# Optimization experiments

Hardware: AMD Instinct MI355X
Metric: run time of the kernel (lower is better)

The kernel has to match this reference:

```python
import jax, jax.numpy as jnp
import numpy as np

G = 8            # group_order
KS = 3           # kernel size
C1, O1 = 1, 16   # gconv1 channels
C2, O2 = 16, 32  # gconv2 channels
HW = 28
NUM_CLASSES = 10


def _bilinear_sample(img, px, py):
    # img: (O, I, K, K); px, py: (K, K) pixel coords; zero padding outside
    # (matches torch grid_sample bilinear, align_corners=False, padding_mode='zeros')
    K = img.shape[-1]
    x0 = jnp.floor(px); y0 = jnp.floor(py)
    wx = px - x0; wy = py - y0
    x0i = x0.astype(jnp.int32); y0i = y0.astype(jnp.int32)

    def gather(yi, xi):
        valid = (yi >= 0) & (yi < K) & (xi >= 0) & (xi < K)
        yc = jnp.clip(yi, 0, K - 1)
        xc = jnp.clip(xi, 0, K - 1)
        return img[:, :, yc, xc] * valid.astype(img.dtype)  # (O,I,K,K)

    return (gather(y0i, x0i) * (1 - wx) * (1 - wy)
            + gather(y0i, x0i + 1) * wx * (1 - wy)
            + gather(y0i + 1, x0i) * (1 - wx) * wy
            + gather(y0i + 1, x0i + 1) * wx * wy)


def _rotated_kernels(base, group_order):
    # Replicates F.affine_grid + F.grid_sample (align_corners=False) for each rotation k.
    K = base.shape[-1]
    coords = (2.0 * jnp.arange(K, dtype=base.dtype) + 1.0) / K - 1.0  # normalized centers
    xs, ys = jnp.meshgrid(coords, coords, indexing='xy')  # x along width, y along height

    def rot_k(k):
        theta = 2.0 * np.pi * k / group_order
        c, s = jnp.cos(theta), jnp.sin(theta)
        gx = c * xs - s * ys   # theta row [cos, -sin, 0]
        gy = s * xs + c * ys   # theta row [sin,  cos, 0]
        px = ((gx + 1.0) * K - 1.0) / 2.0  # unnormalize, align_corners=False
        py = ((gy + 1.0) * K - 1.0) / 2.0
        return _bilinear_sample(base, px, py)

    return jax.vmap(rot_k)(jnp.arange(group_order, dtype=base.dtype))  # (G,O,I,K,K)


def _conv2d(x, w, pad):
    return jax.lax.conv_general_dilated(
        x, w, window_strides=(1, 1), padding=[(pad, pad), (pad, pad)],
        dimension_numbers=('NCHW', 'OIHW', 'NCHW'))


def setup_inputs() -> dict:
    key = jax.random.key(0)
    k1, k2, k3, k4, k5 = jax.random.split(key, 5)
    x = jax.random.normal(k1, (512, C1, HW, HW), dtype=jnp.float32)
    base_weight = jax.random.normal(k2, (O1, C1, KS, KS), dtype=jnp.float32)
    w2 = jax.random.normal(k3, (O2, C2, G, KS, KS), dtype=jnp.float32) * 0.05
    fc_w = jax.random.normal(k4, (NUM_CLASSES, O2 * HW * HW), dtype=jnp.float32) * 0.01
    fc_b = jax.random.normal(k5, (NUM_CLASSES,), dtype=jnp.float32) * 0.01
    return {"x": x, "base_weight": base_weight, "w2": w2, "fc_w": fc_w, "fc_b": fc_b}


def reference(x, base_weight, w2, fc_w, fc_b):
    B = x.shape[0]
    # --- GroupConv2D: steerable rotated kernels, concat along out-channels (k-major) ---
    rk = _rotated_kernels(base_weight, G)           # (G, O1, C1, K, K)
    w1 = rk.reshape(G * O1, C1, KS, KS)
    h = _conv2d(x, w1, 1)                           # (B, G*O1, 28, 28)
    h = jax.nn.relu(h)                              # GroupReLU == plain ReLU

    # --- GroupToGroupConv: circulant structure fused into one conv ---
    # torch: out channel = g*O2 + o (cat dim=1), in channel = c*G + h_idx (view layout)
    g = jnp.arange(G)[:, None]
    hh = jnp.arange(G)[None, :]
    idx = (g - hh) % G                               # (G, G)
    Wc = w2[:, :, idx]                               # (O2, C2, G_g, G_h, K, K)
    Wbig = jnp.transpose(Wc, (2, 0, 1, 3, 4, 5)).reshape(G * O2, C2 * G, KS, KS)
    h2 = _conv2d(h, Wbig, 1)                         # (B, G*O2, 28, 28)
    h2 = jax.nn.relu(h2)

    # --- GroupPooling (mean over the *inner* factor of 8, as in the torch view) ---
    p = h2.reshape(B, (G * O2) // G, G, HW, HW).mean(axis=2)  # (B, 32, 28, 28)

    # --- fc ---
    flat = p.reshape(B, -1)
    return flat @ fc_w.T + fc_b
```

## Files before the change

kernel.cpp:

```cpp
#include <hip/hip_runtime.h>
#include <hip/hip_bf16.h>
#include <cstdint>

#define AS1 __attribute__((address_space(1)))
#define AS3 __attribute__((address_space(3)))

typedef __bf16 bf16x8 __attribute__((ext_vector_type(8)));
typedef float  f32x16 __attribute__((ext_vector_type(16)));

__device__ __forceinline__ void gld_lds16(const void* g, void* l) {
    __builtin_amdgcn_global_load_lds((const AS1 void*)g, (AS3 void*)l, 16, 0, 0);
}

__global__ void k_rot(const float* __restrict__ base, float* __restrict__ w1) {
    int m = threadIdx.x;
    int g = m >> 4, o = m & 15;
    float th = 6.28318530717958647692f * (float)g / 8.0f;
    float c = cosf(th), s = sinf(th);
    for (int i = 0; i < 3; ++i) {
        float ys = (2.0f * i + 1.0f) / 3.0f - 1.0f;
        for (int j = 0; j < 3; ++j) {
            float xs = (2.0f * j + 1.0f) / 3.0f - 1.0f;
            float gx = c * xs - s * ys;
            float gy = s * xs + c * ys;
            float px = ((gx + 1.0f) * 3.0f - 1.0f) * 0.5f;
            float py = ((gy + 1.0f) * 3.0f - 1.0f) * 0.5f;
            float x0 = floorf(px), y0 = floorf(py);
            float wx = px - x0, wy = py - y0;
            int x0i = (int)x0, y0i = (int)y0;
            auto gat = [&](int yi, int xi) -> float {
                bool v = (yi >= 0) && (yi < 3) && (xi >= 0) && (xi < 3);
                int yc = min(max(yi, 0), 2), xc = min(max(xi, 0), 2);
                return v ? base[o * 9 + yc * 3 + xc] : 0.0f;
            };
            w1[m * 9 + i * 3 + j] =
                  gat(y0i, x0i)         * (1.0f - wx) * (1.0f - wy)
                + gat(y0i, x0i + 1)     * wx          * (1.0f - wy)
                + gat(y0i + 1, x0i)     * (1.0f - wx) * wy
                + gat(y0i + 1, x0i + 1) * wx          * wy;
        }
    }
}

__global__ __launch_bounds__(256) void k_conv1(const float* __restrict__ x,
                                               const float* __restrict__ w1g,
                                               const float* __restrict__ w2,
                                               __hip_bfloat16* __restrict__ hl,
                                               __hip_bfloat16* __restrict__ A) {
    int tid = threadIdx.x;

    if (blockIdx.x < 1152) {
        int i = blockIdx.x * 256 + tid;
        int r = i / 1152, k = i - r * 1152;
        int g = r >> 5, o2 = r & 31;
        int kk = k >> 7, cch = k & 127;
        int ky = kk / 3, kx = kk - ky * 3;
        int c2 = cch >> 3, hh = cch & 7;
        int gi = (g - hh) & 7;
        A[i] = __float2bfloat16(w2[((o2 * 16 + c2) * 8 + gi) * 9 + ky * 3 + kx]);
    }

    __shared__ float w1s[1152];
    for (int i = tid; i < 1152; i += 256) w1s[i] = w1g[i];
    __syncthreads();

    const int c0 = (tid & 15) * 8;
    float wreg[8][9];
#pragma unroll
    for (int cc = 0; cc < 8; ++cc)
#pragma unroll
        for (int k = 0; k < 9; ++k) wreg[cc][k] = w1s[(c0 + cc) * 9 + k];

    const int slot = tid >> 4;
    const int band = blockIdx.x % 15;
    const int b    = blockIdx.x / 15;
    const int yy   = band * 2 + (slot >> 3);
    const int xx0  = (slot & 7) * 4;

    const float* xb = x + b * 784;
    float xv[3][6];
#pragma unroll
    for (int t = 0; t < 3; ++t) {
        int sy = yy - 2 + t;
        bool syok = (sy >= 0) && (sy < 28);
#pragma unroll
        for (int u = 0; u < 6; ++u) {
            int sx = xx0 - 2 + u;
            bool ok = syok && (sx >= 0) && (sx < 28);
            xv[t][u] = ok ? xb[sy * 28 + sx] : 0.0f;
        }
    }

    float acc[4][8];
#pragma unroll
    for (int j = 0; j < 4; ++j)
#pragma unroll
        for (int cc = 0; cc < 8; ++cc) acc[j][cc] = 0.0f;

#pragma unroll
    for (int t = 0; t < 3; ++t)
#pragma unroll
        for (int u = 0; u < 3; ++u) {
#pragma unroll
            for (int j = 0; j < 4; ++j) {
                float xvv = xv[t][j + u];
#pragma unroll
                for (int cc = 0; cc < 8; ++cc)
                    acc[j][cc] += xvv * wreg[cc][t * 3 + u];
            }
        }

#pragma unroll
    for (int j = 0; j < 4; ++j) {
        int xx = xx0 + j;
        if (xx < 30) {
            bool interior = (yy >= 1) && (yy <= 28) && (xx >= 1) && (xx <= 28);
            union { __hip_bfloat16 h[8]; float4 f4; } u;
#pragma unroll
            for (int cc = 0; cc < 8; ++cc)
                u.h[cc] = __float2bfloat16(interior ? fmaxf(acc[j][cc], 0.0f) : 0.0f);
            int pi = b * 900 + yy * 30 + xx;
            *(float4*)(hl + (size_t)pi * 128 + c0) = u.f4;
        }
    }
}

__global__ __launch_bounds__(256, 4) void k_conv2(const __hip_bfloat16* __restrict__ A,
                                                  const __hip_bfloat16* __restrict__ hl,
                                                  __hip_bfloat16* __restrict__ p) {
    __shared__ __align__(16) char smem[32768];

    const int tid  = threadIdx.x;
    const int lane = tid & 63;
    const int w    = tid >> 6;
    const int wr   = w >> 1, wc = w & 1;
    const int hi   = lane >> 5;

    const int bid  = blockIdx.x;
    const int xcd  = bid & 7;
    const int slot = bid >> 3;
    const int nt   = xcd + 8 * (slot >> 1);
    const int mt   = slot & 1;
    const int n0 = nt << 7;
    const int r0 = mt << 7;

    uint32_t aG[4], bG[4], ldsOff[4];
#pragma unroll
    for (int q = 0; q < 4; ++q) {
        int ch = w * 4 + q;
        int rl = ch * 8 + (lane >> 3);
        int ca = (lane & 7) ^ (rl & 7) ^ (ch & 3);
        aG[q] = (uint32_t)((r0 + rl) * 2304 + ca * 16);
        int n  = n0 + rl;
        int b  = n / 784; int rr = n - b * 784;
        int y  = rr / 28; int xx = rr - y * 28;
        bG[q]  = (uint32_t)(((b * 30 + y) * 30 + xx) * 256 + ca * 16);
        ldsOff[q] = (uint32_t)(ch * 1024);
    }

    uint32_t aro[2], bro[2]; int asw[2], bsw[2];
#pragma unroll
    for (int t = 0; t < 2; ++t) {
        int rl = 64 * wr + 32 * t + (lane & 31);
        aro[t] = (uint32_t)(rl * 128); asw[t] = (rl & 7) ^ ((rl >> 3) & 3);
        int nl = 64 * wc + 32 * t + (lane & 31);
        bro[t] = (uint32_t)(16384 + nl * 128); bsw[t] = (nl & 7) ^ ((nl >> 3) & 3);
    }

    f32x16 acc[2][2];
#pragma unroll
    for (int i = 0; i < 2; ++i)
#pragma unroll
        for (int j = 0; j < 2; ++j) acc[i][j] = (f32x16)(0.0f);

    const char* Ab = (const char*)A;
    const char* Hb = (const char*)hl;

    for (int s = 0; s < 18; ++s) {
        int kk = s >> 1, half = s & 1;
        int ky = kk / 3, kx = kk - ky * 3;
        int aoff = kk * 256 + half * 128;
        int boff = (ky * 30 + kx) * 256 + half * 128;

        __syncthreads();
#pragma unroll
        for (int q = 0; q < 4; ++q) {
            gld_lds16(Ab + aG[q] + aoff, smem + ldsOff[q]);
            gld_lds16(Hb + bG[q] + boff, smem + 16384 + ldsOff[q]);
        }
        __syncthreads();

#pragma unroll
        for (int kstep = 0; kstep < 4; ++kstep) {
            int cb = kstep * 2 + hi;
            bf16x8 af[2], bf[2];
#pragma unroll
            for (int t = 0; t < 2; ++t) {
                af[t] = *(const bf16x8*)(smem + aro[t] + ((cb ^ asw[t]) * 16));
                bf[t] = *(const bf16x8*)(smem + bro[t] + ((cb ^ bsw[t]) * 16));
            }
#pragma unroll
            for (int i = 0; i < 2; ++i)
#pragma unroll
                for (int j = 0; j < 2; ++j)
                    acc[i][j] = __builtin_amdgcn_mfma_f32_32x32x16_bf16(af[i], bf[j], acc[i][j], 0, 0, 0);
        }
    }

#pragma unroll
    for (int ti = 0; ti < 2; ++ti) {
        int gbase = (r0 + 64 * wr + 32 * ti) >> 3;
#pragma unroll
        for (int tj = 0; tj < 2; ++tj) {
            f32x16 v = acc[ti][tj];
#pragma unroll
            for (int q = 0; q < 4; ++q) {
                float s = fmaxf(v[4*q], 0.0f) + fmaxf(v[4*q+1], 0.0f)
                        + fmaxf(v[4*q+2], 0.0f) + fmaxf(v[4*q+3], 0.0f);
                s += __shfl_xor(s, 32, 64);
                if (hi == 0) {
                    int a = gbase + q;
                    int n = n0 + 64 * wc + 32 * tj + (lane & 31);
                    int b = n / 784; int rr = n - b * 784;
                    p[(b * 32 + a) * 784 + rr] = __float2bfloat16(s * 0.125f);
                }
            }
        }
    }
}

__global__ __launch_bounds__(256) void k_fc(const __hip_bfloat16* __restrict__ p,
                                            const float* __restrict__ fw,
                                            const float* __restrict__ fb,
                                            float* __restrict__ out) {
    int b = blockIdx.x >> 2, ks = blockIdx.x & 3;
    int tid = threadIdx.x;
    const bf16x8* pb = (const bf16x8*)(p + (size_t)b * 25088);
    const float4* w4 = (const float4*)fw;
    float acc[10] = {};
    for (int t = ks * 784 + tid; t < (ks + 1) * 784; t += 256) {
        union { bf16x8 v; __hip_bfloat16 h[8]; } u;
        u.v = pb[t];
        float vf[8];
#pragma unroll
        for (int e = 0; e < 8; ++e) vf[e] = __bfloat162float(u.h[e]);
#pragma unroll
        for (int c = 0; c < 10; ++c) {
            float4 u0 = w4[c * 6272 + 2 * t];
            float4 u1 = w4[c * 6272 + 2 * t + 1];
            acc[c] += vf[0] * u0.x + vf[1] * u0.y + vf[2] * u0.z + vf[3] * u0.w
                    + vf[4] * u1.x + vf[5] * u1.y + vf[6] * u1.z + vf[7] * u1.w;
        }
    }
    __shared__ float red[10][4];
    int lane = tid & 63, wv = tid >> 6;
#pragma unroll
    for (int c = 0; c < 10; ++c) {
        float s = acc[c];
#pragma unroll
        for (int o = 32; o > 0; o >>= 1) s += __shfl_down(s, o, 64);
        if (lane == 0) red[c][wv] = s;
    }
    __syncthreads();
    if (tid < 10) {
        float s = red[tid][0] + red[tid][1] + red[tid][2] + red[tid][3];
        if (ks == 0) s += fb[tid];
        atomicAdd(&out[b * 10 + tid], s);
    }
}

extern "C" void kernel_launch(void* const* d_in, const int* in_sizes, int n_in,
                              void* d_out, int out_size, void* d_ws, size_t ws_size,
                              hipStream_t stream) {
    const float* x  = (const float*)d_in[0];
    const float* bw = (const float*)d_in[1];
    const float* w2 = (const float*)d_in[2];
    const float* fw = (const float*)d_in[3];
    const float* fb = (const float*)d_in[4];
    float* out = (float*)d_out;
    char* ws = (char*)d_ws;

    float*          w1   = (float*)(ws);
    __hip_bfloat16* Amat = (__hip_bfloat16*)(ws + 4608);
    __hip_bfloat16* hl   = (__hip_bfloat16*)(ws + 594432);
    __hip_bfloat16* p    = (__hip_bfloat16*)(ws + 118563328);

    hipMemsetAsync(d_out, 0, (size_t)out_size * sizeof(float), stream);
    k_rot  <<<1,    128, 0, stream>>>(bw, w1);
    k_conv1<<<7680, 256, 0, stream>>>(x, w1, w2, hl, Amat);
    k_conv2<<<6272, 256, 0, stream>>>(Amat, hl, p);
    k_fc   <<<2048, 256, 0, stream>>>(p, fw, fb, out);
}
```

Before: 371.9 us.

## Restructure conv2 GEMM into 256x256 tiles with double-buffered LDS pipeline

Rewrites the second group convolution GEMM so each 512-thread block computes a 256x256 output tile, covering all output channels for 256 pixels. It double-buffers 128KB of LDS and splits each K step into four quadrant phases, so global-to-LDS loads of the next step overlap the MFMAs of the current one. It also uses s_setprio around the MFMA bursts. The larger tile means the pixel operand is fetched once instead of twice, and the pipeline hides load latency that the old two-barrier loop exposed. In exchange, the big LDS footprint limits occupancy and the hand-placed waitcnt/barrier sequencing is fragile.

New measurement: 377.1 us. No clear change (+1.4%).

```diff
diff --git a/kernel.cpp b/kernel.cpp
--- a/kernel.cpp
+++ b/kernel.cpp
@@ -125,104 +125,242 @@
     }
 }
 
-__global__ __launch_bounds__(256, 4) void k_conv2(const __hip_bfloat16* __restrict__ A,
+__global__ __launch_bounds__(512, 2) void k_conv2(const __hip_bfloat16* __restrict__ A,
                                                   const __hip_bfloat16* __restrict__ hl,
                                                   __hip_bfloat16* __restrict__ p) {
-    __shared__ __align__(16) char smem[32768];
+    __shared__ __align__(16) char smem[131072];
 
     const int tid  = threadIdx.x;
     const int lane = tid & 63;
     const int w    = tid >> 6;
-    const int wr   = w >> 1, wc = w & 1;
     const int hi   = lane >> 5;
-
-    const int bid  = blockIdx.x;
-    const int xcd  = bid & 7;
-    const int slot = bid >> 3;
-    const int nt   = xcd + 8 * (slot >> 1);
-    const int mt   = slot & 1;
-    const int n0 = nt << 7;
-    const int r0 = mt << 7;
-
-    uint32_t aG[4], bG[4], ldsOff[4];
-#pragma unroll
-    for (int q = 0; q < 4; ++q) {
-        int ch = w * 4 + q;
+    const int wqr  = w >> 2;
+    const int wqc  = w & 3;
+
+    const int bid = blockIdx.x;
+    const int nt  = (bid & 7) * 196 + (bid >> 3);
+    const int n0  = nt << 8;
+
+    uint32_t aSrc[2], bSrc[2][2], ldsCh[2];
+#pragma unroll
+    for (int q = 0; q < 2; ++q) {
+        int ch = 2 * w + q;
         int rl = ch * 8 + (lane >> 3);
         int ca = (lane & 7) ^ (rl & 7) ^ (ch & 3);
-        aG[q] = (uint32_t)((r0 + rl) * 2304 + ca * 16);
-        int n  = n0 + rl;
-        int b  = n / 784; int rr = n - b * 784;
-        int y  = rr / 28; int xx = rr - y * 28;
-        bG[q]  = (uint32_t)(((b * 30 + y) * 30 + xx) * 256 + ca * 16);
-        ldsOff[q] = (uint32_t)(ch * 1024);
-    }
-
-    uint32_t aro[2], bro[2]; int asw[2], bsw[2];
-#pragma unroll
-    for (int t = 0; t < 2; ++t) {
-        int rl = 64 * wr + 32 * t + (lane & 31);
-        aro[t] = (uint32_t)(rl * 128); asw[t] = (rl & 7) ^ ((rl >> 3) & 3);
-        int nl = 64 * wc + 32 * t + (lane & 31);
-        bro[t] = (uint32_t)(16384 + nl * 128); bsw[t] = (nl & 7) ^ ((nl >> 3) & 3);
-    }
-
-    f32x16 acc[2][2];
-#pragma unroll
-    for (int i = 0; i < 2; ++i)
-#pragma unroll
-        for (int j = 0; j < 2; ++j) acc[i][j] = (f32x16)(0.0f);
+        aSrc[q]  = (uint32_t)(rl * 2304 + ca * 16);
+        ldsCh[q] = (uint32_t)(ch * 1024);
+#pragma unroll
+        for (int hn = 0; hn < 2; ++hn) {
+            int n = n0 + hn * 128 + rl;
+            int b = n / 784; int rr = n - b * 784;
+            int y = rr / 28; int xx = rr - y * 28;
+            bSrc[q][hn] = (uint32_t)(((b * 30 + y) * 30 + xx) * 256 + ca * 16);
+        }
+    }
+
+    uint32_t aRow[2]; int aSwz[2];
+#pragma unroll
+    for (int i = 0; i < 2; ++i) {
+        int r = wqr * 64 + i * 32 + (lane & 31);
+        aRow[i] = (uint32_t)(r * 128);
+        aSwz[i] = (r & 7) ^ ((r >> 3) & 3);
+    }
+    const int rB = wqc * 32 + (lane & 31);
+    const uint32_t bRow = (uint32_t)(rB * 128);
+    const int bSwz = (rB & 7) ^ ((rB >> 3) & 3);
+
+    f32x16 acc[4][2];
+#pragma unroll
+    for (int pq = 0; pq < 4; ++pq)
+#pragma unroll
+        for (int i = 0; i < 2; ++i) acc[pq][i] = (f32x16)(0.0f);
 
     const char* Ab = (const char*)A;
     const char* Hb = (const char*)hl;
 
-    for (int s = 0; s < 18; ++s) {
-        int kk = s >> 1, half = s & 1;
-        int ky = kk / 3, kx = kk - ky * 3;
-        int aoff = kk * 256 + half * 128;
-        int boff = (ky * 30 + kx) * 256 + half * 128;
-
-        __syncthreads();
-#pragma unroll
-        for (int q = 0; q < 4; ++q) {
-            gld_lds16(Ab + aG[q] + aoff, smem + ldsOff[q]);
-            gld_lds16(Hb + bG[q] + boff, smem + 16384 + ldsOff[q]);
-        }
-        __syncthreads();
-
-#pragma unroll
-        for (int kstep = 0; kstep < 4; ++kstep) {
-            int cb = kstep * 2 + hi;
-            bf16x8 af[2], bf[2];
-#pragma unroll
-            for (int t = 0; t < 2; ++t) {
-                af[t] = *(const bf16x8*)(smem + aro[t] + ((cb ^ asw[t]) * 16));
-                bf[t] = *(const bf16x8*)(smem + bro[t] + ((cb ^ bsw[t]) * 16));
-            }
-#pragma unroll
-            for (int i = 0; i < 2; ++i)
-#pragma unroll
-                for (int j = 0; j < 2; ++j)
-                    acc[i][j] = __builtin_amdgcn_mfma_f32_32x32x16_bf16(af[i], bf[j], acc[i][j], 0, 0, 0);
-        }
-    }
-
-#pragma unroll
-    for (int ti = 0; ti < 2; ++ti) {
-        int gbase = (r0 + 64 * wr + 32 * ti) >> 3;
-#pragma unroll
-        for (int tj = 0; tj < 2; ++tj) {
-            f32x16 v = acc[ti][tj];
-#pragma unroll
-            for (int q = 0; q < 4; ++q) {
-                float s = fmaxf(v[4*q], 0.0f) + fmaxf(v[4*q+1], 0.0f)
-                        + fmaxf(v[4*q+2], 0.0f) + fmaxf(v[4*q+3], 0.0f);
-                s += __shfl_xor(s, 32, 64);
+    gld_lds16(Ab + aSrc[0], smem + ldsCh[0]);
+    gld_lds16(Ab + aSrc[1], smem + ldsCh[1]);
+    gld_lds16(Hb + bSrc[0][0], smem + 32768 + ldsCh[0]);
+    gld_lds16(Hb + bSrc[1][0], smem + 32768 + ldsCh[1]);
+    gld_lds16(Hb + bSrc[0][1], smem + 49152 + ldsCh[0]);
+    gld_lds16(Hb + bSrc[1][1], smem + 49152 + ldsCh[1]);
+    gld_lds16(Ab + aSrc[0] + 294912, smem + 16384 + ldsCh[0]);
+    gld_lds16(Ab + aSrc[1] + 294912, smem + 16384 + ldsCh[1]);
+    asm volatile("s_waitcnt vmcnt(4)" ::: "memory");
+    asm volatile("s_barrier" ::: "memory");
+
+#pragma unroll 1
+    for (int t = 0; t < 17; ++t) {
+        const uint32_t cb = (uint32_t)((t & 1) << 16);
+        const uint32_t cn = cb ^ 65536u;
+        const uint32_t aoffn = (uint32_t)((t + 1) * 128);
+        const int kkn = (t + 1) >> 1;
+        const int kyn = kkn / 3;
+        const int kxn = kkn - kyn * 3;
+        const uint32_t boffn = (uint32_t)((kyn * 30 + kxn) * 256 + ((t + 1) & 1) * 128);
+
+        const char* SA0 = smem + cb;
+        const char* SA1 = smem + cb + 16384;
+        const char* SB0 = smem + cb + 32768;
+        const char* SB1 = smem + cb + 49152;
+
+        bf16x8 a0[4], a1[4], bv[4];
+
+#pragma unroll
+        for (int k = 0; k < 4; ++k) {
+            const uint32_t c0 = (uint32_t)(k * 2 + hi);
+            a0[k] = *(const bf16x8*)(SA0 + aRow[0] + ((c0 ^ (uint32_t)aSwz[0]) << 4));
+            a1[k] = *(const bf16x8*)(SA0 + aRow[1] + ((c0 ^ (uint32_t)aSwz[1]) << 4));
+            bv[k] = *(const bf16x8*)(SB0 + bRow    + ((c0 ^ (uint32_t)bSwz ) << 4));
+        }
+        gld_lds16(Ab + aSrc[0] + aoffn, smem + cn + ldsCh[0]);
+        gld_lds16(Ab + aSrc[1] + aoffn, smem + cn + ldsCh[1]);
+        asm volatile("s_barrier" ::: "memory");
+        __builtin_amdgcn_s_setprio(1);
+#pragma unroll
+        for (int k = 0; k < 4; ++k) {
+            acc[0][0] = __builtin_amdgcn_mfma_f32_32x32x16_bf16(a0[k], bv[k], acc[0][0], 0, 0, 0);
+            acc[0][1] = __builtin_amdgcn_mfma_f32_32x32x16_bf16(a1[k], bv[k], acc[0][1], 0, 0, 0);
+        }
+        __builtin_amdgcn_sched_barrier(0);
+        __builtin_amdgcn_s_setprio(0);
+        asm volatile("s_waitcnt vmcnt(4)" ::: "memory");
+        asm volatile("s_barrier" ::: "memory");
+
+#pragma unroll
+        for (int k = 0; k < 4; ++k) {
+            const uint32_t c0 = (uint32_t)(k * 2 + hi);
+            bv[k] = *(const bf16x8*)(SB1 + bRow + ((c0 ^ (uint32_t)bSwz) << 4));
+        }
+        gld_lds16(Hb + bSrc[0][0] + boffn, smem + cn + 32768 + ldsCh[0]);
+        gld_lds16(Hb + bSrc[1][0] + boffn, smem + cn + 32768 + ldsCh[1]);
+        asm volatile("s_barrier" ::: "memory");
+        __builtin_amdgcn_s_setprio(1);
+#pragma unroll
+        for (int k = 0; k < 4; ++k) {
+            acc[1][0] = __builtin_amdgcn_mfma_f32_32x32x16_bf16(a0[k], bv[k], acc[1][0], 0, 0, 0);
+            acc[1][1] = __builtin_amdgcn_mfma_f32_32x32x16_bf16(a1[k], bv[k], acc[1][1], 0, 0, 0);
+        }
+        __builtin_amdgcn_sched_barrier(0);
+        __builtin_amdgcn_s_setprio(0);
+        asm volatile("s_waitcnt vmcnt(4)" ::: "memory");
+        asm volatile("s_barrier" ::: "memory");
+
+#pragma unroll
+        for (int k = 0; k < 4; ++k) {
+            const uint32_t c0 = (uint32_t)(k * 2 + hi);
+            a0[k] = *(const bf16x8*)(SA1 + aRow[0] + ((c0 ^ (uint32_t)aSwz[0]) << 4));
+            a1[k] = *(const bf16x8*)(SA1 + aRow[1] + ((c0 ^ (uint32_t)aSwz[1]) << 4));
+        }
+        gld_lds16(Hb + bSrc[0][1] + boffn, smem + cn + 49152 + ldsCh[0]);
+        gld_lds16(Hb + bSrc[1][1] + boffn, smem + cn + 49152 + ldsCh[1]);
+        asm volatile("s_barrier" ::: "memory");
+        __builtin_amdgcn_s_setprio(1);
+#pragma unroll
+        for (int k = 0; k < 4; ++k) {
+            acc[2][0] = __builtin_amdgcn_mfma_f32_32x32x16_bf16(a0[k], bv[k], acc[2][0], 0, 0, 0);
+            acc[2][1] = __builtin_amdgcn_mfma_f32_32x32x16_bf16(a1[k], bv[k], acc[2][1], 0, 0, 0);
+        }
+        __builtin_amdgcn_sched_barrier(0);
+        __builtin_amdgcn_s_setprio(0);
+        asm volatile("s_barrier" ::: "memory");
+
+#pragma unroll
+        for (int k = 0; k < 4; ++k) {
+            const uint32_t c0 = (uint32_t)(k * 2 + hi);
+            bv[k] = *(const bf16x8*)(SB0 + bRow + ((c0 ^ (uint32_t)bSwz) << 4));
+        }
+        gld_lds16(Ab + aSrc[0] + aoffn + 294912, smem + cn + 16384 + ldsCh[0]);
+        gld_lds16(Ab + aSrc[1] + aoffn + 294912, smem + cn + 16384 + ldsCh[1]);
+        asm volatile("s_barrier" ::: "memory");
+        __builtin_amdgcn_s_setprio(1);
+#pragma unroll
+        for (int k = 0; k < 4; ++k) {
+            acc[3][0] = __builtin_amdgcn_mfma_f32_32x32x16_bf16(a0[k], bv[k], acc[3][0], 0, 0, 0);
+            acc[3][1] = __builtin_amdgcn_mfma_f32_32x32x16_bf16(a1[k], bv[k], acc[3][1], 0, 0, 0);
+        }
+        __builtin_amdgcn_sched_barrier(0);
+        __builtin_amdgcn_s_setprio(0);
+        asm volatile("s_waitcnt vmcnt(4)" ::: "memory");
+        asm volatile("s_barrier" ::: "memory");
+    }
+
+    {
+        const char* SA0 = smem + 65536;
+        const char* SA1 = smem + 65536 + 16384;
+        const char* SB0 = smem + 65536 + 32768;
+        const char* SB1 = smem + 65536 + 49152;
+        bf16x8 a0[4], a1[4], bv[4];
+
+#pragma unroll
+        for (int k = 0; k < 4; ++k) {
+            const uint32_t c0 = (uint32_t)(k * 2 + hi);
+            a0[k] = *(const bf16x8*)(SA0 + aRow[0] + ((c0 ^ (uint32_t)aSwz[0]) << 4));
+            a1[k] = *(const bf16x8*)(SA0 + aRow[1] + ((c0 ^ (uint32_t)aSwz[1]) << 4));
+            bv[k] = *(const bf16x8*)(SB0 + bRow + ((c0 ^ (uint32_t)bSwz) << 4));
+        }
+#pragma unroll
+        for (int k = 0; k < 4; ++k) {
+            acc[0][0] = __builtin_amdgcn_mfma_f32_32x32x16_bf16(a0[k], bv[k], acc[0][0], 0, 0, 0);
+            acc[0][1] = __builtin_amdgcn_mfma_f32_32x32x16_bf16(a1[k], bv[k], acc[0][1], 0, 0, 0);
+        }
+        asm volatile("s_waitcnt vmcnt(2)" ::: "memory");
+        asm volatile("s_barrier" ::: "memory");
+
+#pragma unroll
+        for (int k = 0; k < 4; ++k) {
+            const uint32_t c0 = (uint32_t)(k * 2 + hi);
+            bv[k] = *(const bf16x8*)(SB1 + bRow + ((c0 ^ (uint32_t)bSwz) << 4));
+        }
+#pragma unroll
+        for (int k = 0; k < 4; ++k) {
+            acc[1][0] = __builtin_amdgcn_mfma_f32_32x32x16_bf16(a0[k], bv[k], acc[1][0], 0, 0, 0);
+            acc[1][1] = __builtin_amdgcn_mfma_f32_32x32x16_bf16(a1[k], bv[k], acc[1][1], 0, 0, 0);
+        }
+        asm volatile("s_waitcnt vmcnt(0)" ::: "memory");
+        asm volatile("s_barrier" ::: "memory");
+
+#pragma unroll
+        for (int k = 0; k < 4; ++k) {
+            const uint32_t c0 = (uint32_t)(k * 2 + hi);
+            a0[k] = *(const bf16x8*)(SA1 + aRow[0] + ((c0 ^ (uint32_t)aSwz[0]) << 4));
+            a1[k] = *(const bf16x8*)(SA1 + aRow[1] + ((c0 ^ (uint32_t)aSwz[1]) << 4));
+        }
+#pragma unroll
+        for (int k = 0; k < 4; ++k) {
+            acc[2][0] = __builtin_amdgcn_mfma_f32_32x32x16_bf16(a0[k], bv[k], acc[2][0], 0, 0, 0);
+            acc[2][1] = __builtin_amdgcn_mfma_f32_32x32x16_bf16(a1[k], bv[k], acc[2][1], 0, 0, 0);
+        }
+
+#pragma unroll
+        for (int k = 0; k < 4; ++k) {
+            const uint32_t c0 = (uint32_t)(k * 2 + hi);
+            bv[k] = *(const bf16x8*)(SB0 + bRow + ((c0 ^ (uint32_t)bSwz) << 4));
+        }
+#pragma unroll
+        for (int k = 0; k < 4; ++k) {
+            acc[3][0] = __builtin_amdgcn_mfma_f32_32x32x16_bf16(a0[k], bv[k], acc[3][0], 0, 0, 0);
+            acc[3][1] = __builtin_amdgcn_mfma_f32_32x32x16_bf16(a1[k], bv[k], acc[3][1], 0, 0, 0);
+        }
+    }
+
+    const int QMarr[4] = {0, 0, 1, 1};
+    const int QNarr[4] = {0, 1, 1, 0};
+#pragma unroll
+    for (int pq = 0; pq < 4; ++pq) {
+#pragma unroll
+        for (int i = 0; i < 2; ++i) {
+            f32x16 v = acc[pq][i];
+#pragma unroll
+            for (int u = 0; u < 4; ++u) {
+                float sv = fmaxf(v[4*u], 0.0f) + fmaxf(v[4*u+1], 0.0f)
+                         + fmaxf(v[4*u+2], 0.0f) + fmaxf(v[4*u+3], 0.0f);
+                sv += __shfl_xor(sv, 32, 64);
                 if (hi == 0) {
-                    int a = gbase + q;
-                    int n = n0 + 64 * wc + 32 * tj + (lane & 31);
+                    int a = QMarr[pq] * 16 + wqr * 8 + i * 4 + u;
+                    int n = n0 + QNarr[pq] * 128 + wqc * 32 + (lane & 31);
                     int b = n / 784; int rr = n - b * 784;
-                    p[(b * 32 + a) * 784 + rr] = __float2bfloat16(s * 0.125f);
+                    p[(b * 32 + a) * 784 + rr] = __float2bfloat16(sv * 0.125f);
                 }
             }
         }
@@ -288,6 +426,6 @@
     hipMemsetAsync(d_out, 0, (size_t)out_size * sizeof(float), stream);
     k_rot  <<<1,    128, 0, stream>>>(bw, w1);
     k_conv1<<<7680, 256, 0, stream>>>(x, w1, w2, hl, Amat);
-    k_conv2<<<6272, 256, 0, stream>>>(Amat, hl, p);
+    k_conv2<<<1568, 512, 0, stream>>>(Amat, hl, p);
     k_fc   <<<2048, 256, 0, stream>>>(p, fw, fb, out);
 }
```

## Restructure conv2 GEMM: full-M tiles, register-resident A, double-buffered B

Applied to the files above, without the earlier changes.

The conv2 implicit GEMM now uses 512-thread blocks that each cover all 256 output rows and 256 pixels. The weight (A) fragments are loaded straight from global memory into registers, and the activation (B) tiles are double-buffered in 64KB of LDS. The next tap's B tile is prefetched while the current tap's MFMAs run, which removes one barrier per step and all A traffic through LDS. In exchange the kernel uses more registers and LDS per block, which lowers occupancy, and the grid shrinks to 1568 blocks.

New measurement: 713.0 us. +91.7%, slower.

```diff
diff --git a/kernel.cpp b/kernel.cpp
--- a/kernel.cpp
+++ b/kernel.cpp
@@ -125,104 +125,151 @@
     }
 }
 
-__global__ __launch_bounds__(256, 4) void k_conv2(const __hip_bfloat16* __restrict__ A,
+__global__ __launch_bounds__(512, 2) void k_conv2(const __hip_bfloat16* __restrict__ A,
                                                   const __hip_bfloat16* __restrict__ hl,
                                                   __hip_bfloat16* __restrict__ p) {
-    __shared__ __align__(16) char smem[32768];
+    __shared__ __align__(16) char smem[65536];
 
     const int tid  = threadIdx.x;
     const int lane = tid & 63;
     const int w    = tid >> 6;
-    const int wr   = w >> 1, wc = w & 1;
     const int hi   = lane >> 5;
-
-    const int bid  = blockIdx.x;
-    const int xcd  = bid & 7;
-    const int slot = bid >> 3;
-    const int nt   = xcd + 8 * (slot >> 1);
-    const int mt   = slot & 1;
-    const int n0 = nt << 7;
-    const int r0 = mt << 7;
-
-    uint32_t aG[4], bG[4], ldsOff[4];
-#pragma unroll
-    for (int q = 0; q < 4; ++q) {
-        int ch = w * 4 + q;
+    const int wqr  = w >> 2;
+    const int wqc  = w & 3;
+
+    const int bid = blockIdx.x;
+    const int nt  = (bid & 7) * 196 + (bid >> 3);
+    const int n0  = nt << 8;
+
+    uint32_t bSrc[2][2], ldsCh[2];
+#pragma unroll
+    for (int q = 0; q < 2; ++q) {
+        int ch = 2 * w + q;
         int rl = ch * 8 + (lane >> 3);
         int ca = (lane & 7) ^ (rl & 7) ^ (ch & 3);
-        aG[q] = (uint32_t)((r0 + rl) * 2304 + ca * 16);
-        int n  = n0 + rl;
-        int b  = n / 784; int rr = n - b * 784;
-        int y  = rr / 28; int xx = rr - y * 28;
-        bG[q]  = (uint32_t)(((b * 30 + y) * 30 + xx) * 256 + ca * 16);
-        ldsOff[q] = (uint32_t)(ch * 1024);
-    }
-
-    uint32_t aro[2], bro[2]; int asw[2], bsw[2];
-#pragma unroll
-    for (int t = 0; t < 2; ++t) {
-        int rl = 64 * wr + 32 * t + (lane & 31);
-        aro[t] = (uint32_t)(rl * 128); asw[t] = (rl & 7) ^ ((rl >> 3) & 3);
-        int nl = 64 * wc + 32 * t + (lane & 31);
-        bro[t] = (uint32_t)(16384 + nl * 128); bsw[t] = (nl & 7) ^ ((nl >> 3) & 3);
-    }
-
-    f32x16 acc[2][2];
-#pragma unroll
-    for (int i = 0; i < 2; ++i)
+        ldsCh[q] = (uint32_t)(ch * 1024);
+#pragma unroll
+        for (int hn = 0; hn < 2; ++hn) {
+            int n = n0 + hn * 128 + rl;
+            int b = n / 784; int rr = n - b * 784;
+            int y = rr / 28; int xx = rr - y * 28;
+            bSrc[q][hn] = (uint32_t)(((b * 30 + y) * 30 + xx) * 256 + ca * 16);
+        }
+    }
+
+    uint32_t bRd[2]; int bSw[2];
+#pragma unroll
+    for (int j = 0; j < 2; ++j) {
+        int r = wqc * 64 + j * 32 + (lane & 31);
+        bRd[j] = (uint32_t)((r >> 7) * 16384 + (r & 127) * 128);
+        bSw[j] = (r & 7) ^ ((r >> 3) & 3);
+    }
+
+    const char* aP[4];
+#pragma unroll
+    for (int i = 0; i < 4; ++i) {
+        int row = wqr * 128 + i * 32 + (lane & 31);
+        aP[i] = (const char*)A + (size_t)row * 2304 + hi * 16;
+    }
+
+    f32x16 acc[4][2];
+#pragma unroll
+    for (int i = 0; i < 4; ++i)
 #pragma unroll
         for (int j = 0; j < 2; ++j) acc[i][j] = (f32x16)(0.0f);
 
-    const char* Ab = (const char*)A;
     const char* Hb = (const char*)hl;
 
-    for (int s = 0; s < 18; ++s) {
-        int kk = s >> 1, half = s & 1;
+    auto stageB = [&](int tt, char* dst) {
+        int kk = tt >> 1, half = tt & 1;
         int ky = kk / 3, kx = kk - ky * 3;
-        int aoff = kk * 256 + half * 128;
-        int boff = (ky * 30 + kx) * 256 + half * 128;
-
+        uint32_t boff = (uint32_t)((ky * 30 + kx) * 256 + half * 128);
+        gld_lds16(Hb + bSrc[0][0] + boff, dst + ldsCh[0]);
+        gld_lds16(Hb + bSrc[1][0] + boff, dst + ldsCh[1]);
+        gld_lds16(Hb + bSrc[0][1] + boff, dst + 16384 + ldsCh[0]);
+        gld_lds16(Hb + bSrc[1][1] + boff, dst + 16384 + ldsCh[1]);
+    };
+
+    stageB(0, smem);
+    bf16x8 aT[4][4];
+#pragma unroll
+    for (int ks = 0; ks < 4; ++ks)
+#pragma unroll
+        for (int i = 0; i < 4; ++i)
+            aT[ks][i] = *(const bf16x8*)(aP[i] + ks * 32);
+
+    bf16x8 bEv[2], bOd[2];
+
+#pragma unroll 1
+    for (int t = 0; t < 18; ++t) {
         __syncthreads();
-#pragma unroll
-        for (int q = 0; q < 4; ++q) {
-            gld_lds16(Ab + aG[q] + aoff, smem + ldsOff[q]);
-            gld_lds16(Hb + bG[q] + boff, smem + 16384 + ldsOff[q]);
-        }
-        __syncthreads();
-
-#pragma unroll
-        for (int kstep = 0; kstep < 4; ++kstep) {
-            int cb = kstep * 2 + hi;
-            bf16x8 af[2], bf[2];
-#pragma unroll
-            for (int t = 0; t < 2; ++t) {
-                af[t] = *(const bf16x8*)(smem + aro[t] + ((cb ^ asw[t]) * 16));
-                bf[t] = *(const bf16x8*)(smem + bro[t] + ((cb ^ bsw[t]) * 16));
-            }
-#pragma unroll
-            for (int i = 0; i < 2; ++i)
-#pragma unroll
-                for (int j = 0; j < 2; ++j)
-                    acc[i][j] = __builtin_amdgcn_mfma_f32_32x32x16_bf16(af[i], bf[j], acc[i][j], 0, 0, 0);
-        }
-    }
-
-#pragma unroll
-    for (int ti = 0; ti < 2; ++ti) {
-        int gbase = (r0 + 64 * wr + 32 * ti) >> 3;
-#pragma unroll
-        for (int tj = 0; tj < 2; ++tj) {
-            f32x16 v = acc[ti][tj];
-#pragma unroll
-            for (int q = 0; q < 4; ++q) {
-                float s = fmaxf(v[4*q], 0.0f) + fmaxf(v[4*q+1], 0.0f)
-                        + fmaxf(v[4*q+2], 0.0f) + fmaxf(v[4*q+3], 0.0f);
-                s += __shfl_xor(s, 32, 64);
+        const char* Bb = smem + ((t & 1) << 15);
+        if (t < 17) stageB(t + 1, smem + (((t + 1) & 1) << 15));
+
+#pragma unroll
+        for (int j = 0; j < 2; ++j)
+            bEv[j] = *(const bf16x8*)(Bb + bRd[j] + ((uint32_t)((0 + hi) ^ bSw[j]) << 4));
+#pragma unroll
+        for (int j = 0; j < 2; ++j)
+            bOd[j] = *(const bf16x8*)(Bb + bRd[j] + ((uint32_t)((2 + hi) ^ bSw[j]) << 4));
+
+#pragma unroll
+        for (int i = 0; i < 4; ++i)
+#pragma unroll
+            for (int j = 0; j < 2; ++j)
+                acc[i][j] = __builtin_amdgcn_mfma_f32_32x32x16_bf16(aT[0][i], bEv[j], acc[i][j], 0, 0, 0);
+
+#pragma unroll
+        for (int j = 0; j < 2; ++j)
+            bEv[j] = *(const bf16x8*)(Bb + bRd[j] + ((uint32_t)((4 + hi) ^ bSw[j]) << 4));
+
+#pragma unroll
+        for (int i = 0; i < 4; ++i)
+#pragma unroll
+            for (int j = 0; j < 2; ++j)
+                acc[i][j] = __builtin_amdgcn_mfma_f32_32x32x16_bf16(aT[1][i], bOd[j], acc[i][j], 0, 0, 0);
+
+#pragma unroll
+        for (int j = 0; j < 2; ++j)
+            bOd[j] = *(const bf16x8*)(Bb + bRd[j] + ((uint32_t)((6 + hi) ^ bSw[j]) << 4));
+
+#pragma unroll
+        for (int i = 0; i < 4; ++i)
+#pragma unroll
+            for (int j = 0; j < 2; ++j)
+                acc[i][j] = __builtin_amdgcn_mfma_f32_32x32x16_bf16(aT[2][i], bEv[j], acc[i][j], 0, 0, 0);
+
+#pragma unroll
+        for (int i = 0; i < 4; ++i)
+#pragma unroll
+            for (int j = 0; j < 2; ++j)
+                acc[i][j] = __builtin_amdgcn_mfma_f32_32x32x16_bf16(aT[3][i], bOd[j], acc[i][j], 0, 0, 0);
+
+        if (t < 17) {
+            uint32_t aoffn = (uint32_t)((t + 1) * 128);
+#pragma unroll
+            for (int ks = 0; ks < 4; ++ks)
+#pragma unroll
+                for (int i = 0; i < 4; ++i)
+                    aT[ks][i] = *(const bf16x8*)(aP[i] + aoffn + ks * 32);
+        }
+    }
+
+#pragma unroll
+    for (int i = 0; i < 4; ++i) {
+#pragma unroll
+        for (int j = 0; j < 2; ++j) {
+            f32x16 v = acc[i][j];
+#pragma unroll
+            for (int u = 0; u < 4; ++u) {
+                float sv = fmaxf(v[4*u], 0.0f) + fmaxf(v[4*u+1], 0.0f)
+                         + fmaxf(v[4*u+2], 0.0f) + fmaxf(v[4*u+3], 0.0f);
+                sv += __shfl_xor(sv, 32, 64);
                 if (hi == 0) {
-                    int a = gbase + q;
-                    int n = n0 + 64 * wc + 32 * tj + (lane & 31);
+                    int a = wqr * 16 + i * 4 + u;
+                    int n = n0 + wqc * 64 + j * 32 + (lane & 31);
                     int b = n / 784; int rr = n - b * 784;
-                    p[(b * 32 + a) * 784 + rr] = __float2bfloat16(s * 0.125f);
+                    p[(b * 32 + a) * 784 + rr] = __float2bfloat16(sv * 0.125f);
                 }
             }
         }
@@ -288,6 +335,6 @@
     hipMemsetAsync(d_out, 0, (size_t)out_size * sizeof(float), stream);
     k_rot  <<<1,    128, 0, stream>>>(bw, w1);
     k_conv1<<<7680, 256, 0, stream>>>(x, w1, w2, hl, Amat);
-    k_conv2<<<6272, 256, 0, stream>>>(Amat, hl, p);
+    k_conv2<<<1568, 512, 0, stream>>>(Amat, hl, p);
     k_fc   <<<2048, 256, 0, stream>>>(p, fw, fb, out);
 }
```
